# Kernel tuning notes

Measured on AMD Instinct MI355X. Metric: run time of the kernel, lower is better.

The kernel has to match this reference:

```python
import jax, jax.numpy as jnp
import numpy as np

N_STATE = 8
N_NEURONS = 64
EPS = 1e-4


def setup_inputs() -> dict:
    key = jax.random.key(0)
    ks = jax.random.split(key, 10)
    B = 524288
    return {
        "hidden_state": jax.random.normal(ks[0], (B, N_STATE), dtype=jnp.float32),
        "u": jax.random.normal(ks[1], (B, 6), dtype=jnp.float32),
        "X": jax.random.uniform(ks[2], (2 * N_STATE + N_NEURONS, 2 * N_STATE + N_NEURONS), dtype=jnp.float32),
        "calB_2": jax.random.uniform(ks[3], (N_STATE, 6), dtype=jnp.float32),
        "C_2": jax.random.uniform(ks[4], (5, N_STATE), dtype=jnp.float32),
        "calD_12": jax.random.uniform(ks[5], (N_NEURONS, 6), dtype=jnp.float32),
        "D_21": jax.random.uniform(ks[6], (5, N_NEURONS), dtype=jnp.float32),
        "D_22": jax.random.uniform(ks[7], (5, 6), dtype=jnp.float32),
        "Y_1": jax.random.uniform(ks[8], (N_STATE, N_STATE), dtype=jnp.float32),
        "biasvec": jax.random.uniform(ks[9], (N_STATE + N_NEURONS + 5,), dtype=jnp.float32),
    }


def _system_matrices(X, Y_1):
    s, n = N_STATE, N_NEURONS
    H = X.T @ X + EPS * jnp.eye(2 * s + n, dtype=X.dtype)
    F_ = H[s + n:, :s]
    B1 = H[s + n:, s:s + n]
    calP = H[s + n:, s + n:]
    C1 = -H[s:s + n, :s]
    H11 = H[:s, :s]
    E = 0.5 * (H11 + calP + Y_1)
    H22 = H[s:s + n, s:s + n]
    Lambda = 0.5 * jnp.diag(H22)
    D11 = -jnp.tril(H22, k=-1)
    return E, F_, B1, Lambda, C1, D11


def _calculate_w(x, u, C1, D11, calD_12, Lambda, bw):
    # Dtilde = diag(1/Lambda) @ D11 : strictly lower triangular -> forward substitution
    Dtilde = D11 / Lambda[:, None]
    rhs = x @ C1.T + u @ calD_12.T + bw  # (B, n)
    v0 = rhs / Lambda  # Linv @ rhs row-wise

    def step(v, args):
        i, dcol = args
        vi = jax.lax.dynamic_index_in_dim(v, i, axis=1, keepdims=False)  # (B,)
        return v + jnp.tanh(vi)[:, None] * dcol[None, :], None

    v, _ = jax.lax.scan(step, v0, (jnp.arange(N_NEURONS), Dtilde.T))
    return jnp.tanh(v)


def reference(hidden_state, u, X, calB_2, C_2, calD_12, D_21, D_22, Y_1, biasvec):
    s, n = N_STATE, N_NEURONS
    bx = biasvec[:s]
    bw = biasvec[s:s + n]
    by = biasvec[s + n:]
    E, F_, B1, Lambda, C1, D11 = _system_matrices(X, Y_1)
    Einv = jnp.linalg.inv(E)
    w = _calculate_w(hidden_state, u, C1, D11, calD_12, Lambda, bw)
    Ehidden = hidden_state @ F_.T + w @ B1.T + u @ calB_2.T + bx
    hidden = Ehidden @ Einv.T
    y = hidden_state @ C_2.T + w @ D_21.T + u @ D_22.T + by
    return hidden, y
```

## Files before the change

kernel.cpp:

```cpp
#include <hip/hip_runtime.h>
#include <hip/hip_fp16.h>
#include <math.h>


constexpr int NH = 80;

constexpr int WS_DTT2 = 0;
constexpr int WS_V0C  = 2048;
constexpr int WS_G2P  = 2560;
constexpr int WS_D21P = 2816;
constexpr int WS_G1P  = 2976;
constexpr int WS_G3P  = 3008;
constexpr int WS_C2P  = 3032;
constexpr int WS_D22P = 3052;
constexpr int WS_BWF  = 3072;
constexpr int WS_G4   = 3136;
constexpr int WS_BY   = 3144;
constexpr int WS_H    = 4096;

__device__ __forceinline__ unsigned pack_rn(float a, float b) {
    unsigned lo = __half_as_ushort(__float2half(a));
    unsigned hi = __half_as_ushort(__float2half(b));
    return lo | (hi << 16);
}

typedef _Float16 h2 __attribute__((ext_vector_type(2)));

__device__ __forceinline__ float dot2(unsigned c, unsigned w, float acc) {
#if __has_builtin(__builtin_amdgcn_fdot2)
    return __builtin_amdgcn_fdot2(__builtin_bit_cast(h2, c),
                                  __builtin_bit_cast(h2, w), acc, false);
#else
    float out;
    asm("v_dot2_f32_f16 %0, %1, %2, %3" : "=v"(out) : "v"(c), "v"(w), "0"(acc));
    return out;
#endif
}
__device__ __forceinline__ float lo_f(unsigned u) { return (float)__builtin_bit_cast(h2, u).x; }
__device__ __forceinline__ float hi_f(unsigned u) { return (float)__builtin_bit_cast(h2, u).y; }

__global__ void k_gram(const float* __restrict__ X, float* __restrict__ ws) {
    int idx = blockIdx.x * blockDim.x + threadIdx.x;
    if (idx >= NH * NH) return;
    int a = idx / NH, b = idx % NH;
    float acc = (a == b) ? 1e-4f : 0.f;
    for (int k = 0; k < NH; k++) acc += X[k * NH + a] * X[k * NH + b];
    ws[WS_H + idx] = acc;
}

__global__ void k_prep(const float* __restrict__ calB2,
                       const float* __restrict__ calD12,
                       const float* __restrict__ C2,
                       const float* __restrict__ D21,
                       const float* __restrict__ D22,
                       const float* __restrict__ Y1,
                       const float* __restrict__ bias,
                       float* ws) {
    __shared__ float sM[8][17];
    __shared__ int sPiv;
    __shared__ float srL[64];
    __shared__ float sEinv[64];
    int tid = threadIdx.x;
    const float* H = ws + WS_H;
    unsigned* wsu = (unsigned*)ws;
    const float KAPPA = 2.8853900817779268f;

    if (tid < 128) {
        int r = tid >> 4, c = tid & 15;
        sM[r][c] = (c < 8)
            ? 0.5f * (H[r * NH + c] + H[(72 + r) * NH + 72 + c] + Y1[r * 8 + c])
            : ((c - 8 == r) ? 1.f : 0.f);
    }
    if (tid >= 128 && tid < 192) srL[tid - 128] = 2.0f / H[(8 + tid - 128) * NH + 8 + tid - 128];
    __syncthreads();

    for (int p = 0; p < 8; p++) {
        if (tid == 0) {
            int pr = p; float best = fabsf(sM[p][p]);
            for (int r = p + 1; r < 8; r++) {
                float v = fabsf(sM[r][p]);
                if (v > best) { best = v; pr = r; }
            }
            sPiv = pr;
        }
        __syncthreads();
        int pr = sPiv;
        if (pr != p && tid < 16) { float tv = sM[p][tid]; sM[p][tid] = sM[pr][tid]; sM[pr][tid] = tv; }
        __syncthreads();
        if (tid < 16) {
            float inv = 1.f / sM[p][p];
            sM[p][tid] *= inv;
        }
        __syncthreads();
        float f = 0.f, pc = 0.f;
        if (tid < 128) { int r = tid >> 4, c = tid & 15; f = sM[r][p]; pc = sM[p][c]; }
        __syncthreads();
        if (tid < 128) { int r = tid >> 4, c = tid & 15; if (r != p) sM[r][c] -= f * pc; }
        __syncthreads();
    }
    if (tid < 64) sEinv[tid] = sM[tid >> 3][8 + (tid & 7)];
    __syncthreads();

    for (int idx = tid; idx < 2048; idx += 256) {
        int i = idx >> 5, p = idx & 31;
        int j0 = 2 * p, j1 = 2 * p + 1;
        float f0 = (j0 < i) ? -KAPPA * H[(8 + i) * NH + 8 + j0] * srL[i] : 0.f;
        float f1 = (j1 < i) ? -KAPPA * H[(8 + i) * NH + 8 + j1] * srL[i] : 0.f;
        wsu[WS_DTT2 + idx] = pack_rn(f0, f1);
    }
    for (int idx = tid; idx < 512; idx += 256) {
        int i = idx >> 3, c = idx & 7;
        float f0 = 0.f, f1 = 0.f;
        if (c < 4) {
            f0 = -KAPPA * H[(8 + i) * NH + 2 * c] * srL[i];
            f1 = -KAPPA * H[(8 + i) * NH + 2 * c + 1] * srL[i];
        } else if (c < 7) {
            int d = 2 * (c - 4);
            f0 = KAPPA * calD12[i * 6 + d] * srL[i];
            f1 = KAPPA * calD12[i * 6 + d + 1] * srL[i];
        }
        wsu[WS_V0C + idx] = pack_rn(f0, f1);
    }
    if (tid < 256) {
        int a = tid >> 5, p = tid & 31;
        float g0 = 0.f, g1 = 0.f;
        for (int k = 0; k < 8; k++) {
            g0 += sEinv[a * 8 + k] * H[(72 + k) * NH + 8 + 2 * p];
            g1 += sEinv[a * 8 + k] * H[(72 + k) * NH + 8 + 2 * p + 1];
        }
        wsu[WS_G2P + tid] = pack_rn(g0, g1);
    }
    if (tid < 160) {
        int q = tid / 32, p = tid % 32;
        wsu[WS_D21P + tid] = pack_rn(D21[q * 64 + 2 * p], D21[q * 64 + 2 * p + 1]);
    }
    if (tid < 32) {
        int a = tid >> 2, c = tid & 3;
        float g0 = 0.f, g1 = 0.f;
        for (int k = 0; k < 8; k++) {
            g0 += sEinv[a * 8 + k] * H[(72 + k) * NH + 2 * c];
            g1 += sEinv[a * 8 + k] * H[(72 + k) * NH + 2 * c + 1];
        }
        wsu[WS_G1P + tid] = pack_rn(g0, g1);
    }
    if (tid < 24) {
        int a = tid / 3, c = tid % 3;
        float g0 = 0.f, g1 = 0.f;
        for (int k = 0; k < 8; k++) {
            g0 += sEinv[a * 8 + k] * calB2[k * 6 + 2 * c];
            g1 += sEinv[a * 8 + k] * calB2[k * 6 + 2 * c + 1];
        }
        wsu[WS_G3P + tid] = pack_rn(g0, g1);
    }
    if (tid < 20) {
        int q = tid >> 2, c = tid & 3;
        wsu[WS_C2P + tid] = pack_rn(C2[q * 8 + 2 * c], C2[q * 8 + 2 * c + 1]);
    }
    if (tid < 15) {
        int q = tid / 3, c = tid % 3;
        wsu[WS_D22P + tid] = pack_rn(D22[q * 6 + 2 * c], D22[q * 6 + 2 * c + 1]);
    }
    if (tid < 64) ws[WS_BWF + tid] = KAPPA * bias[8 + tid] * srL[tid];
    if (tid < 8) {
        float acc = 0.f;
        for (int k = 0; k < 8; k++) acc += sEinv[tid * 8 + k] * bias[k];
        ws[WS_G4 + tid] = acc;
    }
    if (tid < 5) ws[WS_BY + tid] = bias[72 + tid];
}

__device__ __forceinline__ float tanh_scaled(float q) {
    float e = __builtin_amdgcn_exp2f(q);
    return 1.f - 2.f * __builtin_amdgcn_rcpf(1.f + e);
}

__global__ __launch_bounds__(256) void k_main(
    const float* __restrict__ xg, const float* __restrict__ ug,
    const float* __restrict__ ws, float* __restrict__ out, int B)
{
    int t = blockIdx.x * blockDim.x + threadIdx.x;
    if (t >= B) return;

    const unsigned* wsu = (const unsigned*)ws;

    unsigned xh[4], uh[3];
    {
        const float4* xp = reinterpret_cast<const float4*>(xg + (size_t)t * 8);
        float4 a0 = xp[0], a1 = xp[1];
        xh[0] = pack_rn(a0.x, a0.y); xh[1] = pack_rn(a0.z, a0.w);
        xh[2] = pack_rn(a1.x, a1.y); xh[3] = pack_rn(a1.z, a1.w);
        const float2* up = reinterpret_cast<const float2*>(ug + (size_t)t * 6);
        float2 c0 = up[0], c1 = up[1], c2 = up[2];
        uh[0] = pack_rn(c0.x, c0.y); uh[1] = pack_rn(c1.x, c1.y); uh[2] = pack_rn(c2.x, c2.y);
    }

    unsigned sv[32];
    #pragma unroll
    for (int k = 0; k < 32; k++) {
        float a0 = ws[WS_BWF + 2 * k];
        float a1 = ws[WS_BWF + 2 * k + 1];
        #pragma unroll
        for (int c = 0; c < 4; c++) {
            a0 = dot2(wsu[WS_V0C + (2 * k) * 8 + c],     xh[c], a0);
            a1 = dot2(wsu[WS_V0C + (2 * k + 1) * 8 + c], xh[c], a1);
        }
        #pragma unroll
        for (int c = 0; c < 3; c++) {
            a0 = dot2(wsu[WS_V0C + (2 * k) * 8 + 4 + c],     uh[c], a0);
            a1 = dot2(wsu[WS_V0C + (2 * k + 1) * 8 + 4 + c], uh[c], a1);
        }
        sv[k] = pack_rn(a0, a1);
    }

    float h[8];
    #pragma unroll
    for (int a = 0; a < 8; a++) {
        float acc = ws[WS_G4 + a];
        #pragma unroll
        for (int c = 0; c < 4; c++) acc = dot2(wsu[WS_G1P + a * 4 + c], xh[c], acc);
        #pragma unroll
        for (int c = 0; c < 3; c++) acc = dot2(wsu[WS_G3P + a * 3 + c], uh[c], acc);
        h[a] = acc;
    }
    float y[5];
    #pragma unroll
    for (int q = 0; q < 5; q++) {
        float acc = ws[WS_BY + q];
        #pragma unroll
        for (int c = 0; c < 4; c++) acc = dot2(wsu[WS_C2P + q * 4 + c], xh[c], acc);
        #pragma unroll
        for (int c = 0; c < 3; c++) acc = dot2(wsu[WS_D22P + q * 3 + c], uh[c], acc);
        y[q] = acc;
    }

    #pragma unroll
    for (int k = 0; k < 32; k++) {
        unsigned cur = sv[k];

        float aE = lo_f(cur), aO = 0.f;
        #pragma unroll
        for (int p = 0; p < k; p += 2) aE = dot2(wsu[WS_DTT2 + (2 * k) * 32 + p], sv[p], aE);
        #pragma unroll
        for (int p = 1; p < k; p += 2) aO = dot2(wsu[WS_DTT2 + (2 * k) * 32 + p], sv[p], aO);
        float we = tanh_scaled(aE + aO);

        float bE = hi_f(cur), bO = 0.f;
        #pragma unroll
        for (int p = 0; p < k; p += 2) bE = dot2(wsu[WS_DTT2 + (2 * k + 1) * 32 + p], sv[p], bE);
        #pragma unroll
        for (int p = 1; p < k; p += 2) bO = dot2(wsu[WS_DTT2 + (2 * k + 1) * 32 + p], sv[p], bO);
        float wo = tanh_scaled(bE + bO + lo_f(wsu[WS_DTT2 + (2 * k + 1) * 32 + k]) * we);

        sv[k] = pack_rn(we, wo);
    }

    #pragma unroll
    for (int a = 0; a < 8; a++) {
        float acc = h[a];
        #pragma unroll
        for (int p = 0; p < 32; p++) acc = dot2(wsu[WS_G2P + a * 32 + p], sv[p], acc);
        h[a] = acc;
    }
    float4* hp = reinterpret_cast<float4*>(out + (size_t)t * 8);
    hp[0] = make_float4(h[0], h[1], h[2], h[3]);
    hp[1] = make_float4(h[4], h[5], h[6], h[7]);

    float* yp = out + (size_t)B * 8 + (size_t)t * 5;
    #pragma unroll
    for (int q = 0; q < 5; q++) {
        float acc = y[q];
        #pragma unroll
        for (int p = 0; p < 32; p++) acc = dot2(wsu[WS_D21P + q * 32 + p], sv[p], acc);
        yp[q] = acc;
    }
}

extern "C" void kernel_launch(void* const* d_in, const int* in_sizes, int n_in,
                              void* d_out, int out_size, void* d_ws, size_t ws_size,
                              hipStream_t stream) {
    const float* x      = (const float*)d_in[0];
    const float* u      = (const float*)d_in[1];
    const float* X      = (const float*)d_in[2];
    const float* calB2  = (const float*)d_in[3];
    const float* C2     = (const float*)d_in[4];
    const float* calD12 = (const float*)d_in[5];
    const float* D21    = (const float*)d_in[6];
    const float* D22    = (const float*)d_in[7];
    const float* Y1     = (const float*)d_in[8];
    const float* bias   = (const float*)d_in[9];
    float* ws  = (float*)d_ws;
    float* out = (float*)d_out;
    int B = in_sizes[0] / 8;

    k_gram<<<(NH * NH + 255) / 256, 256, 0, stream>>>(X, ws);
    k_prep<<<1, 256, 0, stream>>>(calB2, calD12, C2, D21, D22, Y1, bias, ws);
    k_main<<<(B + 255) / 256, 256, 0, stream>>>(x, u, ws, out, B);
}
```

Before: 71.56 us.

## Fuse Gram computation into prep kernel and process two rows per thread

The separate Gram-matrix kernel is folded into the single-block prep kernel: X is staged in shared memory, H = XᵀX is computed there with 2x2 register tiles, and the block grows to 512 threads. This removes one launch and the global round trip for H. The main kernel now has each thread handle two batch rows (t and t+B/2), so every coefficient load from the workspace feeds two dot2 operations and two independent dependency chains can interleave. The cost is roughly double the register pressure and lower occupancy, and odd B would leave the last row unprocessed.

```diff
diff --git a/kernel.cpp b/kernel.cpp
--- a/kernel.cpp
+++ b/kernel.cpp
@@ -16,7 +16,6 @@
 constexpr int WS_BWF  = 3072;
 constexpr int WS_G4   = 3136;
 constexpr int WS_BY   = 3144;
-constexpr int WS_H    = 4096;
 
 __device__ __forceinline__ unsigned pack_rn(float a, float b) {
     unsigned lo = __half_as_ushort(__float2half(a));
@@ -37,41 +36,55 @@
 #endif
 }
 __device__ __forceinline__ float lo_f(unsigned u) { return (float)__builtin_bit_cast(h2, u).x; }
-__device__ __forceinline__ float hi_f(unsigned u) { return (float)__builtin_bit_cast(h2, u).y; }
-
-__global__ void k_gram(const float* __restrict__ X, float* __restrict__ ws) {
-    int idx = blockIdx.x * blockDim.x + threadIdx.x;
-    if (idx >= NH * NH) return;
-    int a = idx / NH, b = idx % NH;
-    float acc = (a == b) ? 1e-4f : 0.f;
-    for (int k = 0; k < NH; k++) acc += X[k * NH + a] * X[k * NH + b];
-    ws[WS_H + idx] = acc;
-}
-
-__global__ void k_prep(const float* __restrict__ calB2,
-                       const float* __restrict__ calD12,
-                       const float* __restrict__ C2,
-                       const float* __restrict__ D21,
-                       const float* __restrict__ D22,
-                       const float* __restrict__ Y1,
-                       const float* __restrict__ bias,
-                       float* ws) {
+
+__global__ __launch_bounds__(512) void k_prep(
+    const float* __restrict__ X,
+    const float* __restrict__ calB2,
+    const float* __restrict__ calD12,
+    const float* __restrict__ C2,
+    const float* __restrict__ D21,
+    const float* __restrict__ D22,
+    const float* __restrict__ Y1,
+    const float* __restrict__ bias,
+    float* ws)
+{
+    __shared__ float sX[NH * NH];
+    __shared__ float sH[NH * NH];
     __shared__ float sM[8][17];
     __shared__ int sPiv;
     __shared__ float srL[64];
     __shared__ float sEinv[64];
     int tid = threadIdx.x;
-    const float* H = ws + WS_H;
     unsigned* wsu = (unsigned*)ws;
     const float KAPPA = 2.8853900817779268f;
+
+    for (int i = tid; i < NH * NH / 4; i += 512)
+        reinterpret_cast<float4*>(sX)[i] = reinterpret_cast<const float4*>(X)[i];
+    __syncthreads();
+
+    for (int idx = tid; idx < 1600; idx += 512) {
+        int ta = idx / 40, tb = idx % 40;
+        int a0 = 2 * ta, b0 = 2 * tb;
+        float s00 = 0.f, s01 = 0.f, s10 = 0.f, s11 = 0.f;
+        for (int k = 0; k < NH; k++) {
+            float xa0 = sX[k * NH + a0], xa1 = sX[k * NH + a0 + 1];
+            float xb0 = sX[k * NH + b0], xb1 = sX[k * NH + b0 + 1];
+            s00 += xa0 * xb0; s01 += xa0 * xb1;
+            s10 += xa1 * xb0; s11 += xa1 * xb1;
+        }
+        if (a0 == b0) { s00 += 1e-4f; s11 += 1e-4f; }
+        sH[a0 * NH + b0] = s00; sH[a0 * NH + b0 + 1] = s01;
+        sH[(a0 + 1) * NH + b0] = s10; sH[(a0 + 1) * NH + b0 + 1] = s11;
+    }
+    __syncthreads();
 
     if (tid < 128) {
         int r = tid >> 4, c = tid & 15;
         sM[r][c] = (c < 8)
-            ? 0.5f * (H[r * NH + c] + H[(72 + r) * NH + 72 + c] + Y1[r * 8 + c])
+            ? 0.5f * (sH[r * NH + c] + sH[(72 + r) * NH + 72 + c] + Y1[r * 8 + c])
             : ((c - 8 == r) ? 1.f : 0.f);
     }
-    if (tid >= 128 && tid < 192) srL[tid - 128] = 2.0f / H[(8 + tid - 128) * NH + 8 + tid - 128];
+    if (tid >= 128 && tid < 192) srL[tid - 128] = 2.0f / sH[(8 + tid - 128) * NH + 8 + tid - 128];
     __syncthreads();
 
     for (int p = 0; p < 8; p++) {
@@ -101,32 +114,32 @@
     if (tid < 64) sEinv[tid] = sM[tid >> 3][8 + (tid & 7)];
     __syncthreads();
 
-    for (int idx = tid; idx < 2048; idx += 256) {
+    for (int idx = tid; idx < 2048; idx += 512) {
         int i = idx >> 5, p = idx & 31;
         int j0 = 2 * p, j1 = 2 * p + 1;
-        float f0 = (j0 < i) ? -KAPPA * H[(8 + i) * NH + 8 + j0] * srL[i] : 0.f;
-        float f1 = (j1 < i) ? -KAPPA * H[(8 + i) * NH + 8 + j1] * srL[i] : 0.f;
+        float f0 = (j0 < i) ? -KAPPA * sH[(8 + i) * NH + 8 + j0] * srL[i] : 0.f;
+        float f1 = (j1 < i) ? -KAPPA * sH[(8 + i) * NH + 8 + j1] * srL[i] : 0.f;
         wsu[WS_DTT2 + idx] = pack_rn(f0, f1);
     }
-    for (int idx = tid; idx < 512; idx += 256) {
-        int i = idx >> 3, c = idx & 7;
+    if (tid < 512) {
+        int i = tid >> 3, c = tid & 7;
         float f0 = 0.f, f1 = 0.f;
         if (c < 4) {
-            f0 = -KAPPA * H[(8 + i) * NH + 2 * c] * srL[i];
-            f1 = -KAPPA * H[(8 + i) * NH + 2 * c + 1] * srL[i];
+            f0 = -KAPPA * sH[(8 + i) * NH + 2 * c] * srL[i];
+            f1 = -KAPPA * sH[(8 + i) * NH + 2 * c + 1] * srL[i];
         } else if (c < 7) {
             int d = 2 * (c - 4);
             f0 = KAPPA * calD12[i * 6 + d] * srL[i];
             f1 = KAPPA * calD12[i * 6 + d + 1] * srL[i];
         }
-        wsu[WS_V0C + idx] = pack_rn(f0, f1);
+        wsu[WS_V0C + tid] = pack_rn(f0, f1);
     }
     if (tid < 256) {
         int a = tid >> 5, p = tid & 31;
         float g0 = 0.f, g1 = 0.f;
         for (int k = 0; k < 8; k++) {
-            g0 += sEinv[a * 8 + k] * H[(72 + k) * NH + 8 + 2 * p];
-            g1 += sEinv[a * 8 + k] * H[(72 + k) * NH + 8 + 2 * p + 1];
+            g0 += sEinv[a * 8 + k] * sH[(72 + k) * NH + 8 + 2 * p];
+            g1 += sEinv[a * 8 + k] * sH[(72 + k) * NH + 8 + 2 * p + 1];
         }
         wsu[WS_G2P + tid] = pack_rn(g0, g1);
     }
@@ -138,8 +151,8 @@
         int a = tid >> 2, c = tid & 3;
         float g0 = 0.f, g1 = 0.f;
         for (int k = 0; k < 8; k++) {
-            g0 += sEinv[a * 8 + k] * H[(72 + k) * NH + 2 * c];
-            g1 += sEinv[a * 8 + k] * H[(72 + k) * NH + 2 * c + 1];
+            g0 += sEinv[a * 8 + k] * sH[(72 + k) * NH + 2 * c];
+            g1 += sEinv[a * 8 + k] * sH[(72 + k) * NH + 2 * c + 1];
         }
         wsu[WS_G1P + tid] = pack_rn(g0, g1);
     }
@@ -179,99 +192,151 @@
     const float* __restrict__ ws, float* __restrict__ out, int B)
 {
     int t = blockIdx.x * blockDim.x + threadIdx.x;
-    if (t >= B) return;
+    int BH = B >> 1;
+    if (t >= BH) return;
+    const int r0 = t, r1 = t + BH;
 
     const unsigned* wsu = (const unsigned*)ws;
 
-    unsigned xh[4], uh[3];
+    unsigned xhA[4], uhA[3], xhB[4], uhB[3];
     {
-        const float4* xp = reinterpret_cast<const float4*>(xg + (size_t)t * 8);
-        float4 a0 = xp[0], a1 = xp[1];
-        xh[0] = pack_rn(a0.x, a0.y); xh[1] = pack_rn(a0.z, a0.w);
-        xh[2] = pack_rn(a1.x, a1.y); xh[3] = pack_rn(a1.z, a1.w);
-        const float2* up = reinterpret_cast<const float2*>(ug + (size_t)t * 6);
-        float2 c0 = up[0], c1 = up[1], c2 = up[2];
-        uh[0] = pack_rn(c0.x, c0.y); uh[1] = pack_rn(c1.x, c1.y); uh[2] = pack_rn(c2.x, c2.y);
-    }
-
-    unsigned sv[32];
+        const float4* xpA = reinterpret_cast<const float4*>(xg + (size_t)r0 * 8);
+        const float4* xpB = reinterpret_cast<const float4*>(xg + (size_t)r1 * 8);
+        float4 a0 = xpA[0], a1 = xpA[1], b0 = xpB[0], b1 = xpB[1];
+        xhA[0] = pack_rn(a0.x, a0.y); xhA[1] = pack_rn(a0.z, a0.w);
+        xhA[2] = pack_rn(a1.x, a1.y); xhA[3] = pack_rn(a1.z, a1.w);
+        xhB[0] = pack_rn(b0.x, b0.y); xhB[1] = pack_rn(b0.z, b0.w);
+        xhB[2] = pack_rn(b1.x, b1.y); xhB[3] = pack_rn(b1.z, b1.w);
+        const float2* upA = reinterpret_cast<const float2*>(ug + (size_t)r0 * 6);
+        const float2* upB = reinterpret_cast<const float2*>(ug + (size_t)r1 * 6);
+        float2 c0 = upA[0], c1 = upA[1], c2 = upA[2];
+        float2 d0 = upB[0], d1 = upB[1], d2 = upB[2];
+        uhA[0] = pack_rn(c0.x, c0.y); uhA[1] = pack_rn(c1.x, c1.y); uhA[2] = pack_rn(c2.x, c2.y);
+        uhB[0] = pack_rn(d0.x, d0.y); uhB[1] = pack_rn(d1.x, d1.y); uhB[2] = pack_rn(d2.x, d2.y);
+    }
+
+    unsigned svA[32], svB[32];
     #pragma unroll
     for (int k = 0; k < 32; k++) {
-        float a0 = ws[WS_BWF + 2 * k];
-        float a1 = ws[WS_BWF + 2 * k + 1];
+        float be = ws[WS_BWF + 2 * k], bo = ws[WS_BWF + 2 * k + 1];
+        float a0 = be, a1 = bo, b0 = be, b1 = bo;
         #pragma unroll
         for (int c = 0; c < 4; c++) {
-            a0 = dot2(wsu[WS_V0C + (2 * k) * 8 + c],     xh[c], a0);
-            a1 = dot2(wsu[WS_V0C + (2 * k + 1) * 8 + c], xh[c], a1);
+            unsigned cE = wsu[WS_V0C + (2 * k) * 8 + c];
+            unsigned cO = wsu[WS_V0C + (2 * k + 1) * 8 + c];
+            a0 = dot2(cE, xhA[c], a0); b0 = dot2(cE, xhB[c], b0);
+            a1 = dot2(cO, xhA[c], a1); b1 = dot2(cO, xhB[c], b1);
         }
         #pragma unroll
         for (int c = 0; c < 3; c++) {
-            a0 = dot2(wsu[WS_V0C + (2 * k) * 8 + 4 + c],     uh[c], a0);
-            a1 = dot2(wsu[WS_V0C + (2 * k + 1) * 8 + 4 + c], uh[c], a1);
-        }
-        sv[k] = pack_rn(a0, a1);
-    }
-
-    float h[8];
+            unsigned cE = wsu[WS_V0C + (2 * k) * 8 + 4 + c];
+            unsigned cO = wsu[WS_V0C + (2 * k + 1) * 8 + 4 + c];
+            a0 = dot2(cE, uhA[c], a0); b0 = dot2(cE, uhB[c], b0);
+            a1 = dot2(cO, uhA[c], a1); b1 = dot2(cO, uhB[c], b1);
+        }
+        svA[k] = pack_rn(a0, a1); svB[k] = pack_rn(b0, b1);
+    }
+
+    float hA[8], hB[8];
     #pragma unroll
     for (int a = 0; a < 8; a++) {
-        float acc = ws[WS_G4 + a];
-        #pragma unroll
-        for (int c = 0; c < 4; c++) acc = dot2(wsu[WS_G1P + a * 4 + c], xh[c], acc);
-        #pragma unroll
-        for (int c = 0; c < 3; c++) acc = dot2(wsu[WS_G3P + a * 3 + c], uh[c], acc);
-        h[a] = acc;
-    }
-    float y[5];
+        float g4 = ws[WS_G4 + a];
+        float accA = g4, accB = g4;
+        #pragma unroll
+        for (int c = 0; c < 4; c++) {
+            unsigned g = wsu[WS_G1P + a * 4 + c];
+            accA = dot2(g, xhA[c], accA); accB = dot2(g, xhB[c], accB);
+        }
+        #pragma unroll
+        for (int c = 0; c < 3; c++) {
+            unsigned g = wsu[WS_G3P + a * 3 + c];
+            accA = dot2(g, uhA[c], accA); accB = dot2(g, uhB[c], accB);
+        }
+        hA[a] = accA; hB[a] = accB;
+    }
+    float yA[5], yB[5];
     #pragma unroll
     for (int q = 0; q < 5; q++) {
-        float acc = ws[WS_BY + q];
-        #pragma unroll
-        for (int c = 0; c < 4; c++) acc = dot2(wsu[WS_C2P + q * 4 + c], xh[c], acc);
-        #pragma unroll
-        for (int c = 0; c < 3; c++) acc = dot2(wsu[WS_D22P + q * 3 + c], uh[c], acc);
-        y[q] = acc;
+        float by = ws[WS_BY + q];
+        float accA = by, accB = by;
+        #pragma unroll
+        for (int c = 0; c < 4; c++) {
+            unsigned g = wsu[WS_C2P + q * 4 + c];
+            accA = dot2(g, xhA[c], accA); accB = dot2(g, xhB[c], accB);
+        }
+        #pragma unroll
+        for (int c = 0; c < 3; c++) {
+            unsigned g = wsu[WS_D22P + q * 3 + c];
+            accA = dot2(g, uhA[c], accA); accB = dot2(g, uhB[c], accB);
+        }
+        yA[q] = accA; yB[q] = accB;
     }
 
     #pragma unroll
     for (int k = 0; k < 32; k++) {
-        unsigned cur = sv[k];
-
-        float aE = lo_f(cur), aO = 0.f;
-        #pragma unroll
-        for (int p = 0; p < k; p += 2) aE = dot2(wsu[WS_DTT2 + (2 * k) * 32 + p], sv[p], aE);
-        #pragma unroll
-        for (int p = 1; p < k; p += 2) aO = dot2(wsu[WS_DTT2 + (2 * k) * 32 + p], sv[p], aO);
-        float we = tanh_scaled(aE + aO);
-
-        float bE = hi_f(cur), bO = 0.f;
-        #pragma unroll
-        for (int p = 0; p < k; p += 2) bE = dot2(wsu[WS_DTT2 + (2 * k + 1) * 32 + p], sv[p], bE);
-        #pragma unroll
-        for (int p = 1; p < k; p += 2) bO = dot2(wsu[WS_DTT2 + (2 * k + 1) * 32 + p], sv[p], bO);
-        float wo = tanh_scaled(bE + bO + lo_f(wsu[WS_DTT2 + (2 * k + 1) * 32 + k]) * we);
-
-        sv[k] = pack_rn(we, wo);
+        unsigned curA = svA[k], curB = svB[k];
+
+        float aE = lo_f(curA), aO = 0.f, bE = lo_f(curB), bO = 0.f;
+        #pragma unroll
+        for (int p = 0; p < k; p += 2) {
+            unsigned c = wsu[WS_DTT2 + (2 * k) * 32 + p];
+            aE = dot2(c, svA[p], aE); bE = dot2(c, svB[p], bE);
+        }
+        #pragma unroll
+        for (int p = 1; p < k; p += 2) {
+            unsigned c = wsu[WS_DTT2 + (2 * k) * 32 + p];
+            aO = dot2(c, svA[p], aO); bO = dot2(c, svB[p], bO);
+        }
+        float weA = tanh_scaled(aE + aO);
+        float weB = tanh_scaled(bE + bO);
+
+        float cE = (float)__builtin_bit_cast(h2, curA).y, cO = 0.f;
+        float dE = (float)__builtin_bit_cast(h2, curB).y, dO = 0.f;
+        #pragma unroll
+        for (int p = 0; p < k; p += 2) {
+            unsigned c = wsu[WS_DTT2 + (2 * k + 1) * 32 + p];
+            cE = dot2(c, svA[p], cE); dE = dot2(c, svB[p], dE);
+        }
+        #pragma unroll
+        for (int p = 1; p < k; p += 2) {
+            unsigned c = wsu[WS_DTT2 + (2 * k + 1) * 32 + p];
+            cO = dot2(c, svA[p], cO); dO = dot2(c, svB[p], dO);
+        }
+        float dcoef = lo_f(wsu[WS_DTT2 + (2 * k + 1) * 32 + k]);
+        float woA = tanh_scaled(cE + cO + dcoef * weA);
+        float woB = tanh_scaled(dE + dO + dcoef * weB);
+
+        svA[k] = pack_rn(weA, woA); svB[k] = pack_rn(weB, woB);
     }
 
     #pragma unroll
     for (int a = 0; a < 8; a++) {
-        float acc = h[a];
-        #pragma unroll
-        for (int p = 0; p < 32; p++) acc = dot2(wsu[WS_G2P + a * 32 + p], sv[p], acc);
-        h[a] = acc;
-    }
-    float4* hp = reinterpret_cast<float4*>(out + (size_t)t * 8);
-    hp[0] = make_float4(h[0], h[1], h[2], h[3]);
-    hp[1] = make_float4(h[4], h[5], h[6], h[7]);
-
-    float* yp = out + (size_t)B * 8 + (size_t)t * 5;
+        float accA = hA[a], accB = hB[a];
+        #pragma unroll
+        for (int p = 0; p < 32; p++) {
+            unsigned g = wsu[WS_G2P + a * 32 + p];
+            accA = dot2(g, svA[p], accA); accB = dot2(g, svB[p], accB);
+        }
+        hA[a] = accA; hB[a] = accB;
+    }
+    float4* hpA = reinterpret_cast<float4*>(out + (size_t)r0 * 8);
+    hpA[0] = make_float4(hA[0], hA[1], hA[2], hA[3]);
+    hpA[1] = make_float4(hA[4], hA[5], hA[6], hA[7]);
+    float4* hpB = reinterpret_cast<float4*>(out + (size_t)r1 * 8);
+    hpB[0] = make_float4(hB[0], hB[1], hB[2], hB[3]);
+    hpB[1] = make_float4(hB[4], hB[5], hB[6], hB[7]);
+
+    float* ypA = out + (size_t)B * 8 + (size_t)r0 * 5;
+    float* ypB = out + (size_t)B * 8 + (size_t)r1 * 5;
     #pragma unroll
     for (int q = 0; q < 5; q++) {
-        float acc = y[q];
-        #pragma unroll
-        for (int p = 0; p < 32; p++) acc = dot2(wsu[WS_D21P + q * 32 + p], sv[p], acc);
-        yp[q] = acc;
+        float accA = yA[q], accB = yB[q];
+        #pragma unroll
+        for (int p = 0; p < 32; p++) {
+            unsigned g = wsu[WS_D21P + q * 32 + p];
+            accA = dot2(g, svA[p], accA); accB = dot2(g, svB[p], accB);
+        }
+        ypA[q] = accA; ypB[q] = accB;
     }
 }
 
@@ -291,8 +356,8 @@
     float* ws  = (float*)d_ws;
     float* out = (float*)d_out;
     int B = in_sizes[0] / 8;
-
-    k_gram<<<(NH * NH + 255) / 256, 256, 0, stream>>>(X, ws);
-    k_prep<<<1, 256, 0, stream>>>(calB2, calD12, C2, D21, D22, Y1, bias, ws);
-    k_main<<<(B + 255) / 256, 256, 0, stream>>>(x, u, ws, out, B);
-}
+    int BH = B >> 1;
+
+    k_prep<<<1, 512, 0, stream>>>(X, calB2, calD12, C2, D21, D22, Y1, bias, ws);
+    k_main<<<(BH + 255) / 256, 256, 0, stream>>>(x, u, ws, out, B);
+}
```

Measured after the change: 71.94 us. Within noise of the previous version (+0.5%).

## Fuse Gram and prep kernels and accumulate outputs inside the recurrence loop

Applied to the files above, without the earlier changes.

Merges the Gram-matrix kernel into the single-block prep kernel. X is staged in shared memory and each thread computes a 4x4 register tile, which removes one launch and the global round trip for H. The 8x8 inverse now uses wavefront shuffles instead of shared-memory Gauss-Jordan passes with many barriers. In the main kernel, the h and y projections are accumulated as each w pair is produced rather than in separate loops afterward, which may shorten live ranges or give more ILP but interleaves extra work into the serial chain.

```diff
diff --git a/kernel.cpp b/kernel.cpp
--- a/kernel.cpp
+++ b/kernel.cpp
@@ -16,7 +16,6 @@
 constexpr int WS_BWF  = 3072;
 constexpr int WS_G4   = 3136;
 constexpr int WS_BY   = 3144;
-constexpr int WS_H    = 4096;
 
 __device__ __forceinline__ unsigned pack_rn(float a, float b) {
     unsigned lo = __half_as_ushort(__float2half(a));
@@ -39,134 +38,152 @@
 __device__ __forceinline__ float lo_f(unsigned u) { return (float)__builtin_bit_cast(h2, u).x; }
 __device__ __forceinline__ float hi_f(unsigned u) { return (float)__builtin_bit_cast(h2, u).y; }
 
-__global__ void k_gram(const float* __restrict__ X, float* __restrict__ ws) {
-    int idx = blockIdx.x * blockDim.x + threadIdx.x;
-    if (idx >= NH * NH) return;
-    int a = idx / NH, b = idx % NH;
-    float acc = (a == b) ? 1e-4f : 0.f;
-    for (int k = 0; k < NH; k++) acc += X[k * NH + a] * X[k * NH + b];
-    ws[WS_H + idx] = acc;
-}
-
-__global__ void k_prep(const float* __restrict__ calB2,
-                       const float* __restrict__ calD12,
-                       const float* __restrict__ C2,
-                       const float* __restrict__ D21,
-                       const float* __restrict__ D22,
-                       const float* __restrict__ Y1,
-                       const float* __restrict__ bias,
-                       float* ws) {
-    __shared__ float sM[8][17];
-    __shared__ int sPiv;
-    __shared__ float srL[64];
+__global__ __launch_bounds__(512) void k_prep(
+    const float* __restrict__ X,
+    const float* __restrict__ calB2,
+    const float* __restrict__ calD12,
+    const float* __restrict__ C2,
+    const float* __restrict__ D21,
+    const float* __restrict__ D22,
+    const float* __restrict__ Y1,
+    const float* __restrict__ bias,
+    float* ws)
+{
+    __shared__ float sX[NH * NH];
+    __shared__ float sH[NH * NH];
     __shared__ float sEinv[64];
+    __shared__ float sLam[64];
     int tid = threadIdx.x;
-    const float* H = ws + WS_H;
     unsigned* wsu = (unsigned*)ws;
     const float KAPPA = 2.8853900817779268f;
 
-    if (tid < 128) {
-        int r = tid >> 4, c = tid & 15;
-        sM[r][c] = (c < 8)
-            ? 0.5f * (H[r * NH + c] + H[(72 + r) * NH + 72 + c] + Y1[r * 8 + c])
-            : ((c - 8 == r) ? 1.f : 0.f);
-    }
-    if (tid >= 128 && tid < 192) srL[tid - 128] = 2.0f / H[(8 + tid - 128) * NH + 8 + tid - 128];
+    for (int i = tid; i < NH * NH / 4; i += 512)
+        reinterpret_cast<float4*>(sX)[i] = reinterpret_cast<const float4*>(X)[i];
     __syncthreads();
 
-    for (int p = 0; p < 8; p++) {
-        if (tid == 0) {
-            int pr = p; float best = fabsf(sM[p][p]);
-            for (int r = p + 1; r < 8; r++) {
-                float v = fabsf(sM[r][p]);
-                if (v > best) { best = v; pr = r; }
+    if (tid < 400) {
+        int ta = tid / 20, tb = tid % 20;
+        int a0 = 4 * ta, b0 = 4 * tb;
+        float acc[4][4];
+        #pragma unroll
+        for (int i = 0; i < 4; i++)
+            #pragma unroll
+            for (int j = 0; j < 4; j++) acc[i][j] = 0.f;
+        for (int k = 0; k < NH; k++) {
+            float4 xa = *reinterpret_cast<const float4*>(&sX[k * NH + a0]);
+            float4 xb = *reinterpret_cast<const float4*>(&sX[k * NH + b0]);
+            float av[4] = { xa.x, xa.y, xa.z, xa.w };
+            float bv[4] = { xb.x, xb.y, xb.z, xb.w };
+            #pragma unroll
+            for (int i = 0; i < 4; i++)
+                #pragma unroll
+                for (int j = 0; j < 4; j++) acc[i][j] += av[i] * bv[j];
+        }
+        #pragma unroll
+        for (int i = 0; i < 4; i++) {
+            #pragma unroll
+            for (int j = 0; j < 4; j++) {
+                float v = acc[i][j];
+                if (ta == tb && i == j) v += 1e-4f;
+                sH[(a0 + i) * NH + b0 + j] = v;
             }
-            sPiv = pr;
-        }
-        __syncthreads();
-        int pr = sPiv;
-        if (pr != p && tid < 16) { float tv = sM[p][tid]; sM[p][tid] = sM[pr][tid]; sM[pr][tid] = tv; }
-        __syncthreads();
-        if (tid < 16) {
-            float inv = 1.f / sM[p][p];
-            sM[p][tid] *= inv;
-        }
-        __syncthreads();
-        float f = 0.f, pc = 0.f;
-        if (tid < 128) { int r = tid >> 4, c = tid & 15; f = sM[r][p]; pc = sM[p][c]; }
-        __syncthreads();
-        if (tid < 128) { int r = tid >> 4, c = tid & 15; if (r != p) sM[r][c] -= f * pc; }
-        __syncthreads();
-    }
-    if (tid < 64) sEinv[tid] = sM[tid >> 3][8 + (tid & 7)];
+        }
+    }
     __syncthreads();
 
-    for (int idx = tid; idx < 2048; idx += 256) {
+    if (tid < 64) {
+        int r = tid >> 3, c = tid & 7;
+        float vm = 0.5f * (sH[r * NH + c] + sH[(72 + r) * NH + 72 + c] + Y1[r * 8 + c]);
+        float vi = (r == c) ? 1.f : 0.f;
+        for (int p = 0; p < 8; p++) {
+            int pr = p; float best = -1.f;
+            for (int r2 = p; r2 < 8; r2++) {
+                float cand = fabsf(__shfl(vm, r2 * 8 + p, 64));
+                if (cand > best) { best = cand; pr = r2; }
+            }
+            int srcr = (r == p) ? pr : ((r == pr) ? p : r);
+            vm = __shfl(vm, srcr * 8 + c, 64);
+            vi = __shfl(vi, srcr * 8 + c, 64);
+            float pivv = __shfl(vm, p * 8 + p, 64);
+            float inv = 1.0f / pivv;
+            if (r == p) { vm *= inv; vi *= inv; }
+            float fm = __shfl(vm, r * 8 + p, 64);
+            float pm = __shfl(vm, p * 8 + c, 64);
+            float pi = __shfl(vi, p * 8 + c, 64);
+            if (r != p) { vm -= fm * pm; vi -= fm * pi; }
+        }
+        sEinv[tid] = vi;
+    } else if (tid < 128) {
+        int i = tid - 64;
+        sLam[i] = 2.0f / sH[(8 + i) * NH + 8 + i];
+    } else {
+        int idx = tid - 128;
+        if (idx < 160) {
+            int q = idx / 32, p = idx % 32;
+            wsu[WS_D21P + idx] = pack_rn(D21[q * 64 + 2 * p], D21[q * 64 + 2 * p + 1]);
+        } else if (idx < 180) {
+            int j = idx - 160, q = j >> 2, c = j & 3;
+            wsu[WS_C2P + j] = pack_rn(C2[q * 8 + 2 * c], C2[q * 8 + 2 * c + 1]);
+        } else if (idx < 195) {
+            int j = idx - 180, q = j / 3, c = j % 3;
+            wsu[WS_D22P + j] = pack_rn(D22[q * 6 + 2 * c], D22[q * 6 + 2 * c + 1]);
+        } else if (idx < 200) {
+            ws[WS_BY + idx - 195] = bias[72 + idx - 195];
+        }
+    }
+    __syncthreads();
+
+    for (int idx = tid; idx < 2048; idx += 512) {
         int i = idx >> 5, p = idx & 31;
         int j0 = 2 * p, j1 = 2 * p + 1;
-        float f0 = (j0 < i) ? -KAPPA * H[(8 + i) * NH + 8 + j0] * srL[i] : 0.f;
-        float f1 = (j1 < i) ? -KAPPA * H[(8 + i) * NH + 8 + j1] * srL[i] : 0.f;
+        float f0 = (j0 < i) ? -KAPPA * sH[(8 + i) * NH + 8 + j0] * sLam[i] : 0.f;
+        float f1 = (j1 < i) ? -KAPPA * sH[(8 + i) * NH + 8 + j1] * sLam[i] : 0.f;
         wsu[WS_DTT2 + idx] = pack_rn(f0, f1);
     }
-    for (int idx = tid; idx < 512; idx += 256) {
-        int i = idx >> 3, c = idx & 7;
+    {
+        int i = tid >> 3, c = tid & 7;
         float f0 = 0.f, f1 = 0.f;
         if (c < 4) {
-            f0 = -KAPPA * H[(8 + i) * NH + 2 * c] * srL[i];
-            f1 = -KAPPA * H[(8 + i) * NH + 2 * c + 1] * srL[i];
+            f0 = -KAPPA * sH[(8 + i) * NH + 2 * c] * sLam[i];
+            f1 = -KAPPA * sH[(8 + i) * NH + 2 * c + 1] * sLam[i];
         } else if (c < 7) {
             int d = 2 * (c - 4);
-            f0 = KAPPA * calD12[i * 6 + d] * srL[i];
-            f1 = KAPPA * calD12[i * 6 + d + 1] * srL[i];
-        }
-        wsu[WS_V0C + idx] = pack_rn(f0, f1);
-    }
+            f0 = KAPPA * calD12[i * 6 + d] * sLam[i];
+            f1 = KAPPA * calD12[i * 6 + d + 1] * sLam[i];
+        }
+        wsu[WS_V0C + tid] = pack_rn(f0, f1);
+    }
+    if (tid < 64) ws[WS_BWF + tid] = KAPPA * bias[8 + tid] * sLam[tid];
     if (tid < 256) {
         int a = tid >> 5, p = tid & 31;
         float g0 = 0.f, g1 = 0.f;
         for (int k = 0; k < 8; k++) {
-            g0 += sEinv[a * 8 + k] * H[(72 + k) * NH + 8 + 2 * p];
-            g1 += sEinv[a * 8 + k] * H[(72 + k) * NH + 8 + 2 * p + 1];
+            g0 += sEinv[a * 8 + k] * sH[(72 + k) * NH + 8 + 2 * p];
+            g1 += sEinv[a * 8 + k] * sH[(72 + k) * NH + 8 + 2 * p + 1];
         }
         wsu[WS_G2P + tid] = pack_rn(g0, g1);
-    }
-    if (tid < 160) {
-        int q = tid / 32, p = tid % 32;
-        wsu[WS_D21P + tid] = pack_rn(D21[q * 64 + 2 * p], D21[q * 64 + 2 * p + 1]);
-    }
-    if (tid < 32) {
-        int a = tid >> 2, c = tid & 3;
+    } else if (tid < 288) {
+        int j = tid - 256, a = j >> 2, c = j & 3;
         float g0 = 0.f, g1 = 0.f;
         for (int k = 0; k < 8; k++) {
-            g0 += sEinv[a * 8 + k] * H[(72 + k) * NH + 2 * c];
-            g1 += sEinv[a * 8 + k] * H[(72 + k) * NH + 2 * c + 1];
-        }
-        wsu[WS_G1P + tid] = pack_rn(g0, g1);
-    }
-    if (tid < 24) {
-        int a = tid / 3, c = tid % 3;
+            g0 += sEinv[a * 8 + k] * sH[(72 + k) * NH + 2 * c];
+            g1 += sEinv[a * 8 + k] * sH[(72 + k) * NH + 2 * c + 1];
+        }
+        wsu[WS_G1P + j] = pack_rn(g0, g1);
+    } else if (tid < 312) {
+        int j = tid - 288, a = j / 3, c = j % 3;
         float g0 = 0.f, g1 = 0.f;
         for (int k = 0; k < 8; k++) {
             g0 += sEinv[a * 8 + k] * calB2[k * 6 + 2 * c];
             g1 += sEinv[a * 8 + k] * calB2[k * 6 + 2 * c + 1];
         }
-        wsu[WS_G3P + tid] = pack_rn(g0, g1);
-    }
-    if (tid < 20) {
-        int q = tid >> 2, c = tid & 3;
-        wsu[WS_C2P + tid] = pack_rn(C2[q * 8 + 2 * c], C2[q * 8 + 2 * c + 1]);
-    }
-    if (tid < 15) {
-        int q = tid / 3, c = tid % 3;
-        wsu[WS_D22P + tid] = pack_rn(D22[q * 6 + 2 * c], D22[q * 6 + 2 * c + 1]);
-    }
-    if (tid < 64) ws[WS_BWF + tid] = KAPPA * bias[8 + tid] * srL[tid];
-    if (tid < 8) {
+        wsu[WS_G3P + j] = pack_rn(g0, g1);
+    } else if (tid < 320) {
+        int a = tid - 312;
         float acc = 0.f;
-        for (int k = 0; k < 8; k++) acc += sEinv[tid * 8 + k] * bias[k];
-        ws[WS_G4 + tid] = acc;
-    }
-    if (tid < 5) ws[WS_BY + tid] = bias[72 + tid];
+        for (int k = 0; k < 8; k++) acc += sEinv[a * 8 + k] * bias[k];
+        ws[WS_G4 + a] = acc;
+    }
 }
 
 __device__ __forceinline__ float tanh_scaled(float q) {
@@ -251,28 +268,22 @@
         for (int p = 1; p < k; p += 2) bO = dot2(wsu[WS_DTT2 + (2 * k + 1) * 32 + p], sv[p], bO);
         float wo = tanh_scaled(bE + bO + lo_f(wsu[WS_DTT2 + (2 * k + 1) * 32 + k]) * we);
 
-        sv[k] = pack_rn(we, wo);
-    }
-
-    #pragma unroll
-    for (int a = 0; a < 8; a++) {
-        float acc = h[a];
-        #pragma unroll
-        for (int p = 0; p < 32; p++) acc = dot2(wsu[WS_G2P + a * 32 + p], sv[p], acc);
-        h[a] = acc;
-    }
+        unsigned wk = pack_rn(we, wo);
+        sv[k] = wk;
+
+        #pragma unroll
+        for (int a = 0; a < 8; a++) h[a] = dot2(wsu[WS_G2P + a * 32 + k], wk, h[a]);
+        #pragma unroll
+        for (int q = 0; q < 5; q++) y[q] = dot2(wsu[WS_D21P + q * 32 + k], wk, y[q]);
+    }
+
     float4* hp = reinterpret_cast<float4*>(out + (size_t)t * 8);
     hp[0] = make_float4(h[0], h[1], h[2], h[3]);
     hp[1] = make_float4(h[4], h[5], h[6], h[7]);
 
     float* yp = out + (size_t)B * 8 + (size_t)t * 5;
     #pragma unroll
-    for (int q = 0; q < 5; q++) {
-        float acc = y[q];
-        #pragma unroll
-        for (int p = 0; p < 32; p++) acc = dot2(wsu[WS_D21P + q * 32 + p], sv[p], acc);
-        yp[q] = acc;
-    }
+    for (int q = 0; q < 5; q++) yp[q] = y[q];
 }
 
 extern "C" void kernel_launch(void* const* d_in, const int* in_sizes, int n_in,
@@ -292,7 +303,6 @@
     float* out = (float*)d_out;
     int B = in_sizes[0] / 8;
 
-    k_gram<<<(NH * NH + 255) / 256, 256, 0, stream>>>(X, ws);
-    k_prep<<<1, 256, 0, stream>>>(calB2, calD12, C2, D21, D22, Y1, bias, ws);
+    k_prep<<<1, 512, 0, stream>>>(X, calB2, calD12, C2, D21, D22, Y1, bias, ws);
     k_main<<<(B + 255) / 256, 256, 0, stream>>>(x, u, ws, out, B);
 }
```

Result: slower. 75.27 us (+5.2%).
